# Kernel optimization log

Hardware: AMD Instinct MI355X
Metric: run time of the kernel (lower is better)

The kernel has to match this reference:

```python
import jax, jax.numpy as jnp
import numpy as np

HIDDEN = 1024
INTER = 4096
NUM_EXPERTS = 8
TOP_K = 2
NUM_TOKENS = 8192


def setup_inputs() -> dict:
    key = jax.random.key(0)
    k_x, k_r, k_w1, k_w2 = jax.random.split(key, 4)
    x = jax.random.normal(k_x, (NUM_TOKENS, HIDDEN), dtype=jnp.float32)
    router_w = jax.random.normal(k_r, (NUM_EXPERTS, HIDDEN), dtype=jnp.float32) * 0.02
    expert_w1 = jax.random.normal(k_w1, (NUM_EXPERTS, HIDDEN, INTER), dtype=jnp.float32) * 0.02
    # torch init: std = 0.02 / sqrt(2 * num_experts)
    expert_w2 = jax.random.normal(k_w2, (NUM_EXPERTS, INTER, HIDDEN), dtype=jnp.float32) * (0.02 / (2 * NUM_EXPERTS) ** 0.5)
    return {"x": x, "router_w": router_w, "expert_w1": expert_w1, "expert_w2": expert_w2}


def reference(x, router_w, expert_w1, expert_w2):
    num_tokens = x.shape[0]
    # Router: logits -> softmax -> top-k -> renormalize (matches torch.topk on probs)
    router_logits = x @ router_w.T                      # [T, E]
    probs = jax.nn.softmax(router_logits, axis=-1)       # [T, E]
    top_vals, top_idx = jax.lax.top_k(probs, TOP_K)      # [T, K]
    top_vals = top_vals / jnp.sum(top_vals, axis=-1, keepdims=True)

    # Auxiliary load-balancing loss (uses only the top-1 expert, as in torch code)
    expert_mask = jax.nn.one_hot(top_idx[:, 0], NUM_EXPERTS, dtype=x.dtype)  # [T, E]
    tokens_per_expert = expert_mask.sum(axis=0)                              # [E]
    router_prob = probs.mean(axis=0)                                         # [E]
    aux_loss = jnp.sum(tokens_per_expert / num_tokens * router_prob) * NUM_EXPERTS

    # Per-token combine weight for each expert (scatter top-k weights to dense [T, E])
    combine = jnp.zeros((num_tokens, NUM_EXPERTS), dtype=x.dtype)
    combine = combine.at[jnp.arange(num_tokens)[:, None], top_idx].add(top_vals)

    # Per-expert 2-layer MLP (silu), weighted combine. Loop over fixed small E.
    output = jnp.zeros_like(x)
    for e in range(NUM_EXPERTS):
        h = jax.nn.silu(x @ expert_w1[e])            # [T, I]
        output = output + combine[:, e:e + 1] * (h @ expert_w2[e])
    return output, aux_loss
```

## Files before the change

kernel.cpp:

```cpp
#include <hip/hip_runtime.h>
#include <hip/hip_bf16.h>
#include <stdint.h>

#define NTOK  8192
#define HID   1024
#define INTER 4096
#define NEXP  8
#define NSLOT (NTOK * 2)

typedef __attribute__((ext_vector_type(4))) float f32x4;
typedef __attribute__((ext_vector_type(8))) short bf16x8;
typedef __attribute__((ext_vector_type(4))) short bf16x4;

__device__ __forceinline__ short f2bf(float f) {
  union { float f; uint32_t u; } v; v.f = f;
  uint32_t u = v.u;
  u += 0x7FFFu + ((u >> 16) & 1u);
  return (short)(u >> 16);
}

__device__ __forceinline__ void glds16(const short* g, short* l) {
  __builtin_amdgcn_global_load_lds(
      (const __attribute__((address_space(1))) void*)g,
      (__attribute__((address_space(3))) void*)l, 16, 0, 0);
}

__global__ __launch_bounds__(256) void castx_k(const float* __restrict__ in,
                                               short* __restrict__ out) {
  size_t i = ((size_t)blockIdx.x * 256 + threadIdx.x) * 4;
  f32x4 v = *(const f32x4*)(in + i);
  bf16x4 o = { f2bf(v.x), f2bf(v.y), f2bf(v.z), f2bf(v.w) };
  *(bf16x4*)(out + i) = o;
}

__global__ __launch_bounds__(256) void router_k(
    const float* __restrict__ x, const float* __restrict__ rw,
    int* __restrict__ top_idx, float* __restrict__ top_w,
    float* __restrict__ probsum, float* __restrict__ cnt1) {
  __shared__ float lrw[NEXP * HID];
  __shared__ float red[4][2 * NEXP];
  int tid = threadIdx.x;
  for (int i = tid * 4; i < NEXP * HID; i += 1024)
    *(f32x4*)(lrw + i) = *(const f32x4*)(rw + i);
  __syncthreads();
  int lane = tid & 63;
  int wv = tid >> 6;
  float pacc[NEXP], cacc[NEXP];
#pragma unroll
  for (int e = 0; e < NEXP; e++) { pacc[e] = 0.f; cacc[e] = 0.f; }
#pragma unroll
  for (int it = 0; it < 4; it++) {
    int t = blockIdx.x * 16 + it * 4 + wv;
    const float* xr = x + (size_t)t * HID;
    float acc[NEXP];
#pragma unroll
    for (int e = 0; e < NEXP; e++) acc[e] = 0.f;
#pragma unroll
    for (int k4 = 0; k4 < 4; k4++) {
      int k = k4 * 256 + lane * 4;
      f32x4 xv = *(const f32x4*)(xr + k);
#pragma unroll
      for (int e = 0; e < NEXP; e++) {
        f32x4 rv = *(const f32x4*)(lrw + e * HID + k);
        acc[e] += xv.x * rv.x + xv.y * rv.y + xv.z * rv.z + xv.w * rv.w;
      }
    }
#pragma unroll
    for (int e = 0; e < NEXP; e++) {
#pragma unroll
      for (int off = 32; off > 0; off >>= 1)
        acc[e] += __shfl_xor(acc[e], off);
    }
    float mx = acc[0];
#pragma unroll
    for (int e = 1; e < NEXP; e++) mx = fmaxf(mx, acc[e]);
    float p[NEXP], s = 0.f;
#pragma unroll
    for (int e = 0; e < NEXP; e++) { p[e] = expf(acc[e] - mx); s += p[e]; }
    float inv = 1.f / s;
    float p1 = -1.f, p2 = -1.f; int i1 = 0, i2 = 0;
#pragma unroll
    for (int e = 0; e < NEXP; e++) {
      float pe = p[e] * inv;
      p[e] = pe;
      if (pe > p1)      { p2 = p1; i2 = i1; p1 = pe; i1 = e; }
      else if (pe > p2) { p2 = pe; i2 = e; }
    }
    if (lane == 0) {
      float rs = 1.f / (p1 + p2);
      top_idx[t * 2] = i1; top_idx[t * 2 + 1] = i2;
      top_w[t * 2] = p1 * rs; top_w[t * 2 + 1] = p2 * rs;
#pragma unroll
      for (int e = 0; e < NEXP; e++) {
        pacc[e] += p[e];
        cacc[e] += (i1 == e) ? 1.f : 0.f;
      }
    }
  }
  if (lane == 0) {
#pragma unroll
    for (int e = 0; e < NEXP; e++) {
      red[wv][e] = pacc[e];
      red[wv][NEXP + e] = cacc[e];
    }
  }
  __syncthreads();
  if (tid < NEXP) {
    float s = 0.f, c = 0.f;
#pragma unroll
    for (int w = 0; w < 4; w++) { s += red[w][tid]; c += red[w][NEXP + tid]; }
    atomicAdd(&probsum[tid], s);
    atomicAdd(&cnt1[tid], c);
  }
}

__global__ void aux_k(const float* probsum, const float* cnt1, float* out_aux) {
  if (threadIdx.x == 0 && blockIdx.x == 0) {
    float s = 0.f;
    for (int e = 0; e < NEXP; e++) s += cnt1[e] * probsum[e];
    out_aux[0] = s * (float)NEXP / ((float)NTOK * (float)NTOK);
  }
}

__global__ void lists_k(const int* __restrict__ top_idx, int* __restrict__ cnt,
                        int* __restrict__ lists) {
  int i = blockIdx.x * 256 + threadIdx.x;
  if (i < NSLOT) {
    int e = top_idx[i];
    int pos = atomicAdd(cnt + e, 1);
    lists[e * NTOK + pos] = i;
  }
}

__global__ __launch_bounds__(256) void transpose_k(
    const float* __restrict__ in, short* __restrict__ out, int K, int N) {
  __shared__ short tile[64][72];
  int e = blockIdx.z;
  in  += (size_t)e * K * N;
  out += (size_t)e * K * N;
  int n0 = blockIdx.x * 64, k0 = blockIdx.y * 64;
  int tid = threadIdx.x;
#pragma unroll
  for (int i = 0; i < 4; i++) {
    int k = (tid >> 4) + i * 16;
    int c = (tid & 15) * 4;
    f32x4 v = *(const f32x4*)(in + (size_t)(k0 + k) * N + n0 + c);
    tile[k][c] = f2bf(v.x); tile[k][c + 1] = f2bf(v.y);
    tile[k][c + 2] = f2bf(v.z); tile[k][c + 3] = f2bf(v.w);
  }
  __syncthreads();
#pragma unroll
  for (int i = 0; i < 2; i++) {
    int cid = tid + i * 256;
    int n = cid >> 3, kk = (cid & 7) * 8;
    bf16x8 o;
#pragma unroll
    for (int j = 0; j < 8; j++) o[j] = tile[kk + j][n];
    *(bf16x8*)(out + (size_t)(n0 + n) * K + k0 + kk) = o;
  }
}

template <int KDIM, int NDIM, bool L1>
__global__ __launch_bounds__(256) void moe_gemm_k(
    const short* __restrict__ A, const short* __restrict__ Bt,
    void* __restrict__ outp, const int* __restrict__ cnt,
    const int* __restrict__ lists, const float* __restrict__ top_w) {
  constexpr int NB = NDIM / 128;
  constexpr int MB = NTOK / 128;
  constexpr int NWG = NB * MB * NEXP;
  int id = blockIdx.x;
  id = (id & 7) * (NWG >> 3) + (id >> 3);
  int n = id % NB;
  int rem = id / NB;
  int m = rem % MB;
  int e = rem / MB;

  int ce = cnt[e];
  int m0 = m * 128;
  if (m0 >= ce) return;
  int n0 = n * 128;
  const int* list = lists + e * NTOK;
  const short* B = Bt + (size_t)e * (size_t)NDIM * KDIM;

  __shared__ short As[2][128 * 32];
  __shared__ short Bs[2][128 * 32];
  __shared__ int   sSlot[128];
  __shared__ float sW[128];

  int tid = threadIdx.x;
  if (tid < 128) {
    int idx = m0 + tid;
    if (idx >= ce) idx = ce - 1;
    int slot = list[idx];
    sSlot[tid] = slot;
    sW[tid] = L1 ? 0.f : top_w[slot];
  }
  __syncthreads();

  int r1 = tid >> 2, cs = tid & 3;
  int r2 = r1 + 64;
  int q1 = (cs ^ ((r1 >> 1) & 3)) * 8;
  int q2 = (cs ^ ((r2 >> 1) & 3)) * 8;
  int ar1 = L1 ? (sSlot[r1] >> 1) : sSlot[r1];
  int ar2 = L1 ? (sSlot[r2] >> 1) : sSlot[r2];
  const short* gA1 = A + (size_t)ar1 * KDIM + q1;
  const short* gA2 = A + (size_t)ar2 * KDIM + q2;
  const short* gB1 = B + (size_t)(n0 + r1) * KDIM + q1;
  const short* gB2 = B + (size_t)(n0 + r2) * KDIM + q2;

  int lane = tid & 63, wave = tid >> 6;
  int wm = wave & 1, wn = wave >> 1;
  int lr = lane & 15, quad = lane >> 4;
  int aoff[4], boff[4];
#pragma unroll
  for (int mi = 0; mi < 4; mi++) {
    int r = wm * 64 + mi * 16 + lr;
    aoff[mi] = r * 32 + (quad ^ ((r >> 1) & 3)) * 8;
  }
#pragma unroll
  for (int ni = 0; ni < 4; ni++) {
    int nn = wn * 64 + ni * 16 + lr;
    boff[ni] = nn * 32 + (quad ^ ((nn >> 1) & 3)) * 8;
  }

  f32x4 acc[4][4] = {};

#define STAGE(buf, ko)                                  \
  do {                                                  \
    glds16(gA1 + (ko), As[buf] + tid * 8);              \
    glds16(gA2 + (ko), As[buf] + 2048 + tid * 8);       \
    glds16(gB1 + (ko), Bs[buf] + tid * 8);              \
    glds16(gB2 + (ko), Bs[buf] + 2048 + tid * 8);       \
  } while (0)

#define COMPUTE(buf)                                                          \
  do {                                                                        \
    bf16x8 af[4], bfg[4];                                                     \
    _Pragma("unroll")                                                         \
    for (int mi = 0; mi < 4; mi++) af[mi] = *(const bf16x8*)(As[buf] + aoff[mi]); \
    _Pragma("unroll")                                                         \
    for (int ni = 0; ni < 4; ni++) bfg[ni] = *(const bf16x8*)(Bs[buf] + boff[ni]); \
    _Pragma("unroll")                                                         \
    for (int mi = 0; mi < 4; mi++)                                            \
      _Pragma("unroll")                                                       \
      for (int ni = 0; ni < 4; ni++)                                          \
        acc[mi][ni] = __builtin_amdgcn_mfma_f32_16x16x32_bf16(af[mi], bfg[ni], acc[mi][ni], 0, 0, 0); \
  } while (0)

  constexpr int NK = KDIM / 32;
  STAGE(0, 0);
  __syncthreads();
  for (int kt = 0; kt < NK; kt += 2) {
    STAGE(1, (kt + 1) * 32);
    COMPUTE(0);
    __syncthreads();
    if (kt + 2 < NK) STAGE(0, (kt + 2) * 32);
    COMPUTE(1);
    __syncthreads();
  }
#undef STAGE
#undef COMPUTE

  int ncol0 = n0 + wn * 64 + lr;
#pragma unroll
  for (int mi = 0; mi < 4; mi++) {
#pragma unroll
    for (int rg = 0; rg < 4; rg++) {
      int r = wm * 64 + mi * 16 + quad * 4 + rg;
      int gm = m0 + r;
      if (gm < ce) {
        int slot = sSlot[r];
#pragma unroll
        for (int ni = 0; ni < 4; ni++) {
          float v = acc[mi][ni][rg];
          int col = ncol0 + ni * 16;
          if (L1) {
            float sv = v / (1.f + expf(-v));
            ((short*)outp)[(size_t)slot * NDIM + col] = f2bf(sv);
          } else {
            atomicAdd((float*)outp + (size_t)(slot >> 1) * NDIM + col, v * sW[r]);
          }
        }
      }
    }
  }
}

extern "C" void kernel_launch(void* const* d_in, const int* in_sizes, int n_in,
                              void* d_out, int out_size, void* d_ws, size_t ws_size,
                              hipStream_t stream) {
  const float* x  = (const float*)d_in[0];
  const float* rw = (const float*)d_in[1];
  const float* w1 = (const float*)d_in[2];
  const float* w2 = (const float*)d_in[3];
  float* out = (float*)d_out;

  char* ws = (char*)d_ws;
  size_t off = 0;
  auto alloc = [&](size_t b) { void* p = ws + off; off += (b + 255) & ~(size_t)255; return p; };
  short* wt    = (short*)alloc((size_t)NEXP * HID * INTER * 2);
  short* h     = (short*)alloc((size_t)NSLOT * INTER * 2);
  short* xb    = (short*)alloc((size_t)NTOK * HID * 2);
  int*   tidx  = (int*)alloc(NSLOT * 4);
  float* tw    = (float*)alloc(NSLOT * 4);
  int*   lists = (int*)alloc(NEXP * NTOK * 4);
  int*   cnt   = (int*)alloc(256);
  float* probsum = (float*)(cnt + 8);
  float* cnt1    = (float*)(cnt + 16);

  hipMemsetAsync(cnt, 0, 256, stream);
  hipMemsetAsync(out, 0, (size_t)out_size * 4, stream);

  castx_k<<<(NTOK * HID / 4) / 256, 256, 0, stream>>>(x, xb);
  router_k<<<NTOK / 16, 256, 0, stream>>>(x, rw, tidx, tw, probsum, cnt1);
  aux_k<<<1, 64, 0, stream>>>(probsum, cnt1, out + (size_t)NTOK * HID);
  lists_k<<<NSLOT / 256, 256, 0, stream>>>(tidx, cnt, lists);

  transpose_k<<<dim3(INTER / 64, HID / 64, NEXP), 256, 0, stream>>>(w1, wt, HID, INTER);
  moe_gemm_k<HID, INTER, true>
      <<<(INTER / 128) * (NTOK / 128) * NEXP, 256, 0, stream>>>(
          xb, wt, h, cnt, lists, tw);

  transpose_k<<<dim3(HID / 64, INTER / 64, NEXP), 256, 0, stream>>>(w2, wt, INTER, HID);
  moe_gemm_k<INTER, HID, false>
      <<<(HID / 128) * (NTOK / 128) * NEXP, 256, 0, stream>>>(
          h, wt, out, cnt, lists, tw);
}
```

Measured before the change: 869.9 us.

## Enlarge MoE GEMM tiles to 256x256 with 512 threads and restructured pipeline

```diff
diff --git a/kernel.cpp b/kernel.cpp
--- a/kernel.cpp
+++ b/kernel.cpp
@@ -161,12 +161,12 @@
 }
 
 template <int KDIM, int NDIM, bool L1>
-__global__ __launch_bounds__(256) void moe_gemm_k(
+__global__ __launch_bounds__(512, 2) void moe_gemm_k(
     const short* __restrict__ A, const short* __restrict__ Bt,
     void* __restrict__ outp, const int* __restrict__ cnt,
     const int* __restrict__ lists, const float* __restrict__ top_w) {
-  constexpr int NB = NDIM / 128;
-  constexpr int MB = NTOK / 128;
+  constexpr int NB = NDIM / 256;
+  constexpr int MB = NTOK / 256;
   constexpr int NWG = NB * MB * NEXP;
   int id = blockIdx.x;
   id = (id & 7) * (NWG >> 3) + (id >> 3);
@@ -176,19 +176,19 @@
   int e = rem / MB;
 
   int ce = cnt[e];
-  int m0 = m * 128;
+  int m0 = m * 256;
   if (m0 >= ce) return;
-  int n0 = n * 128;
+  int n0 = n * 256;
   const int* list = lists + e * NTOK;
   const short* B = Bt + (size_t)e * (size_t)NDIM * KDIM;
 
-  __shared__ short As[2][128 * 32];
-  __shared__ short Bs[2][128 * 32];
-  __shared__ int   sSlot[128];
-  __shared__ float sW[128];
+  __shared__ short As[2 * 256 * 32];
+  __shared__ short Bs[2 * 256 * 32];
+  __shared__ int   sSlot[256];
+  __shared__ float sW[256];
 
   int tid = threadIdx.x;
-  if (tid < 128) {
+  if (tid < 256) {
     int idx = m0 + tid;
     if (idx >= ce) idx = ce - 1;
     int slot = list[idx];
@@ -198,7 +198,7 @@
   __syncthreads();
 
   int r1 = tid >> 2, cs = tid & 3;
-  int r2 = r1 + 64;
+  int r2 = r1 + 128;
   int q1 = (cs ^ ((r1 >> 1) & 3)) * 8;
   int q2 = (cs ^ ((r2 >> 1) & 3)) * 8;
   int ar1 = L1 ? (sSlot[r1] >> 1) : sSlot[r1];
@@ -211,10 +211,10 @@
   int lane = tid & 63, wave = tid >> 6;
   int wm = wave & 1, wn = wave >> 1;
   int lr = lane & 15, quad = lane >> 4;
-  int aoff[4], boff[4];
-#pragma unroll
-  for (int mi = 0; mi < 4; mi++) {
-    int r = wm * 64 + mi * 16 + lr;
+  int aoff[8], boff[4];
+#pragma unroll
+  for (int mi = 0; mi < 8; mi++) {
+    int r = wm * 128 + mi * 16 + lr;
     aoff[mi] = r * 32 + (quad ^ ((r >> 1) & 3)) * 8;
   }
 #pragma unroll
@@ -223,50 +223,59 @@
     boff[ni] = nn * 32 + (quad ^ ((nn >> 1) & 3)) * 8;
   }
 
-  f32x4 acc[4][4] = {};
-
-#define STAGE(buf, ko)                                  \
-  do {                                                  \
-    glds16(gA1 + (ko), As[buf] + tid * 8);              \
-    glds16(gA2 + (ko), As[buf] + 2048 + tid * 8);       \
-    glds16(gB1 + (ko), Bs[buf] + tid * 8);              \
-    glds16(gB2 + (ko), Bs[buf] + 2048 + tid * 8);       \
+  f32x4 acc[8][4] = {};
+
+#define STAGE(BUF, KO)                                          \
+  do {                                                          \
+    glds16(gA1 + (KO), As + (BUF) * 8192 + tid * 8);            \
+    glds16(gA2 + (KO), As + (BUF) * 8192 + 4096 + tid * 8);     \
+    glds16(gB1 + (KO), Bs + (BUF) * 8192 + tid * 8);            \
+    glds16(gB2 + (KO), Bs + (BUF) * 8192 + 4096 + tid * 8);     \
   } while (0)
 
-#define COMPUTE(buf)                                                          \
+#define KBODY(BUF, MORE, STG_T)                                               \
   do {                                                                        \
-    bf16x8 af[4], bfg[4];                                                     \
+    bf16x8 af[8], bfg[4];                                                     \
     _Pragma("unroll")                                                         \
-    for (int mi = 0; mi < 4; mi++) af[mi] = *(const bf16x8*)(As[buf] + aoff[mi]); \
+    for (int mi = 0; mi < 8; mi++)                                            \
+      af[mi] = *(const bf16x8*)(As + (BUF) * 8192 + aoff[mi]);                \
     _Pragma("unroll")                                                         \
-    for (int ni = 0; ni < 4; ni++) bfg[ni] = *(const bf16x8*)(Bs[buf] + boff[ni]); \
+    for (int ni = 0; ni < 4; ni++)                                            \
+      bfg[ni] = *(const bf16x8*)(Bs + (BUF) * 8192 + boff[ni]);               \
+    asm volatile("s_waitcnt lgkmcnt(0)\n\ts_barrier" ::: "memory");           \
+    if (MORE) STAGE(BUF, (STG_T) * 32);                                       \
+    __builtin_amdgcn_s_setprio(1);                                            \
     _Pragma("unroll")                                                         \
-    for (int mi = 0; mi < 4; mi++)                                            \
+    for (int mi = 0; mi < 8; mi++)                                            \
       _Pragma("unroll")                                                       \
       for (int ni = 0; ni < 4; ni++)                                          \
         acc[mi][ni] = __builtin_amdgcn_mfma_f32_16x16x32_bf16(af[mi], bfg[ni], acc[mi][ni], 0, 0, 0); \
+    __builtin_amdgcn_s_setprio(0);                                            \
   } while (0)
 
   constexpr int NK = KDIM / 32;
   STAGE(0, 0);
-  __syncthreads();
+  STAGE(1, 32);
+  asm volatile("s_waitcnt vmcnt(4)\n\ts_barrier" ::: "memory");
+
+#pragma unroll 1
   for (int kt = 0; kt < NK; kt += 2) {
-    STAGE(1, (kt + 1) * 32);
-    COMPUTE(0);
-    __syncthreads();
-    if (kt + 2 < NK) STAGE(0, (kt + 2) * 32);
-    COMPUTE(1);
-    __syncthreads();
-  }
+    bool more = (kt + 2 < NK);
+    KBODY(0, more, kt + 2);
+    if (more) asm volatile("s_waitcnt vmcnt(4)\n\ts_barrier" ::: "memory");
+    else      asm volatile("s_waitcnt vmcnt(0)\n\ts_barrier" ::: "memory");
+    KBODY(1, more, kt + 3);
+    if (more) asm volatile("s_waitcnt vmcnt(4)\n\ts_barrier" ::: "memory");
+  }
+#undef KBODY
 #undef STAGE
-#undef COMPUTE
 
   int ncol0 = n0 + wn * 64 + lr;
 #pragma unroll
-  for (int mi = 0; mi < 4; mi++) {
+  for (int mi = 0; mi < 8; mi++) {
 #pragma unroll
     for (int rg = 0; rg < 4; rg++) {
-      int r = wm * 64 + mi * 16 + quad * 4 + rg;
+      int r = wm * 128 + mi * 16 + quad * 4 + rg;
       int gm = m0 + r;
       if (gm < ce) {
         int slot = sSlot[r];
@@ -318,11 +327,11 @@
 
   transpose_k<<<dim3(INTER / 64, HID / 64, NEXP), 256, 0, stream>>>(w1, wt, HID, INTER);
   moe_gemm_k<HID, INTER, true>
-      <<<(INTER / 128) * (NTOK / 128) * NEXP, 256, 0, stream>>>(
+      <<<(INTER / 256) * (NTOK / 256) * NEXP, 512, 0, stream>>>(
           xb, wt, h, cnt, lists, tw);
 
   transpose_k<<<dim3(HID / 64, INTER / 64, NEXP), 256, 0, stream>>>(w2, wt, INTER, HID);
   moe_gemm_k<INTER, HID, false>
-      <<<(HID / 128) * (NTOK / 128) * NEXP, 256, 0, stream>>>(
+      <<<(HID / 256) * (NTOK / 256) * NEXP, 512, 0, stream>>>(
           h, wt, out, cnt, lists, tw);
 }
```

Result: slower. 900.7 us (+3.5%).
